# Kernel optimization log

Hardware: AMD Instinct MI355X
Metric: run time of the kernel (lower is better)

Reference implementation:

```python
import jax, jax.numpy as jnp
import numpy as np


def setup_inputs() -> dict:
    key = jax.random.key(0)
    kq, kk, kv = jax.random.split(key, 3)
    B, L, H, E = 2, 2048, 16, 64
    queries = jax.random.normal(kq, (B, L, H, E), dtype=jnp.float32)
    keys = jax.random.normal(kk, (B, L, H, E), dtype=jnp.float32)
    values = jax.random.normal(kv, (B, L, H, E), dtype=jnp.float32)
    return {"queries": queries, "keys": keys, "values": values}


def reference(queries, keys, values):
    # queries: [B, L, H, E], keys: [B, S, H, E], values: [B, S, H, D]
    B, L, H, E = queries.shape
    S = keys.shape[1]
    scale = 1.0 / jnp.sqrt(jnp.asarray(E, dtype=queries.dtype))
    # scores: [B, H, L, S]
    scores = jnp.einsum('blhe,bshe->bhls', queries, keys)
    # TriangularCausalMask: mask out strictly-upper-triangular (future) positions
    causal = jnp.triu(jnp.ones((L, S), dtype=bool), k=1)
    neg_inf = jnp.asarray(-jnp.inf, dtype=scores.dtype)
    scores = jnp.where(causal[None, None, :, :], neg_inf, scores)
    A = jax.nn.softmax(scale * scores, axis=-1)  # dropout p=0.0 (eval)
    # V: [B, L, H, D]
    V = jnp.einsum('bhls,bshd->blhd', A, values)
    return V
```

## Files before the change

kernel.cpp:

```cpp
#include <hip/hip_runtime.h>


constexpr int LL = 2048, HH = 16;
constexpr float SL2E = 0.125f * 1.44269504088896340736f;
constexpr float NEG = -1e30f;
constexpr size_t PLANE = 262144;

using bf16x8 = __attribute__((ext_vector_type(8))) short;
using f32x4  = __attribute__((ext_vector_type(4))) float;

__device__ inline float fast_exp2(float x) { return __builtin_amdgcn_exp2f(x); }

__device__ inline unsigned short f2bf(float f) {
    unsigned u = __builtin_bit_cast(unsigned, f);
    return (unsigned short)((u + 0x7fffu + ((u >> 16) & 1u)) >> 16);
}
__device__ inline unsigned pk2r(float lo, float hi) {
    unsigned al = __builtin_bit_cast(unsigned, lo) + 0x8000u;
    unsigned ah = __builtin_bit_cast(unsigned, hi) + 0x8000u;
    return __builtin_amdgcn_perm(ah, al, 0x07060302u);
}
__device__ inline void gload16(const void* g, void* l) {
    __builtin_amdgcn_global_load_lds(
        (const __attribute__((address_space(1))) unsigned int*)g,
        (__attribute__((address_space(3))) unsigned int*)l, 16, 0, 0);
}

__global__ __launch_bounds__(256) void prepack(
    const float* __restrict__ K, const float* __restrict__ V,
    char* __restrict__ wsK, char* __restrict__ wsV)
{
    const int bh = blockIdx.x >> 4;
    const int chunk = blockIdx.x & 15;
    const int b = bh >> 4, h = bh & 15;
    const int s0 = chunk * 128;
    const int tid = threadIdx.x;
    const int wv = tid >> 6, lane = tid & 63;
    const int g = lane >> 4, c16 = lane & 15;

    char* outK = wsK + (size_t)bh * PLANE;
    char* outV = wsV + (size_t)bh * PLANE;

    #pragma unroll
    for (int i = 0; i < 4; ++i) {
        const int idx = i * 256 + tid;
        const int sl = idx >> 3, o = idx & 7;
        const float* src = K + (((size_t)(b * 2048 + s0 + sl)) * 16 + h) * 64 + o * 8;
        float4 f0 = *(const float4*)src;
        float4 f1 = *(const float4*)(src + 4);
        short4 lo = make_short4((short)f2bf(f0.x), (short)f2bf(f0.y),
                                (short)f2bf(f0.z), (short)f2bf(f0.w));
        short4 hi = make_short4((short)f2bf(f1.x), (short)f2bf(f1.y),
                                (short)f2bf(f1.z), (short)f2bf(f1.w));
        char* dst = outK + (s0 + sl) * 128 + ((o << 4) ^ ((sl & 7) << 4));
        *(short4*)dst = lo;
        *(short4*)(dst + 8) = hi;
    }

    const int vrow0 = wv * 4 + g;
    const float* pV = V + (((size_t)(b * 2048 + s0 + vrow0)) * 16 + h) * 64 + c16 * 4;
    const int d = c16 * 4 + g;
    #pragma unroll
    for (int it = 0; it < 8; ++it) {
        float4 vf = *(const float4*)(pV + (size_t)it * 16 * 1024);
        unsigned short a0 = f2bf(vf.x), a1 = f2bf(vf.y),
                       a2 = f2bf(vf.z), a3 = f2bf(vf.w);
        unsigned s1 = (g & 1) ? ((unsigned)a0 | ((unsigned)a2 << 16))
                              : ((unsigned)a1 | ((unsigned)a3 << 16));
        unsigned r1 = __shfl_xor(s1, 16, 64);
        if (g & 1) { a0 = (unsigned short)r1; a2 = (unsigned short)(r1 >> 16); }
        else       { a1 = (unsigned short)r1; a3 = (unsigned short)(r1 >> 16); }
        unsigned s2 = (g & 2) ? ((unsigned)a0 | ((unsigned)a1 << 16))
                              : ((unsigned)a2 | ((unsigned)a3 << 16));
        unsigned r2 = __shfl_xor(s2, 32, 64);
        if (g & 2) { a0 = (unsigned short)r2; a1 = (unsigned short)(r2 >> 16); }
        else       { a2 = (unsigned short)r2; a3 = (unsigned short)(r2 >> 16); }
        const int p_g  = 4 * (it >> 1) + wv;
        const int half = it & 1;
        char* dst = outV + (size_t)d * 4096 + chunk * 256
                  + (((p_g ^ (d & 7)) << 4) + (half << 3));
        *(short4*)dst = make_short4((short)a0, (short)a1, (short)a2, (short)a3);
    }
}

__global__ __launch_bounds__(256, 2) void attn_main(
    const float* __restrict__ Q, const char* __restrict__ wsK,
    const char* __restrict__ wsV, float* __restrict__ Out)
{
    __shared__ __align__(16) short Kb[2][8192];
    __shared__ __align__(16) short Vt[2][8192];

    const int tid  = threadIdx.x;
    const int wv   = tid >> 6;
    const int lane = tid & 63;
    const int g    = lane >> 4;
    const int c16  = lane & 15;
    const int wq   = wv >> 1;
    const int wk   = wv & 1;

    const int i  = blockIdx.x;
    const int bh = ((i & 7) << 2) | ((i >> 3) & 3);
    const int qslot = i >> 5;
    const int qi = (qslot < 8) ? (15 - qslot) : (qslot - 8);
    const int b = bh >> 4, h = bh & 15;
    const int q0  = qi * 128;
    const int wqb = q0 + wq * 64;

    bf16x8 bQ[4][2];
    #pragma unroll
    for (int qg = 0; qg < 4; ++qg) {
        const int qrow = wqb + qg * 16 + c16;
        const float* qp = Q + ((size_t)(b * LL + qrow) * HH + h) * 64 + g * 8;
        #pragma unroll
        for (int es = 0; es < 2; ++es) {
            float4 f0 = *(const float4*)(qp + es * 32);
            float4 f1 = *(const float4*)(qp + es * 32 + 4);
            bf16x8 a;
            a[0] = f2bf(f0.x * SL2E); a[1] = f2bf(f0.y * SL2E);
            a[2] = f2bf(f0.z * SL2E); a[3] = f2bf(f0.w * SL2E);
            a[4] = f2bf(f1.x * SL2E); a[5] = f2bf(f1.y * SL2E);
            a[6] = f2bf(f1.z * SL2E); a[7] = f2bf(f1.w * SL2E);
            bQ[qg][es] = a;
        }
    }

    const short ONE = (short)0x3F80;
    const bf16x8 bOnes = {ONE, ONE, ONE, ONE, ONE, ONE, ONE, ONE};

    const char* planeK = wsK + (size_t)bh * PLANE;
    const char* planeV = wsV + (size_t)bh * PLANE;

    f32x4 Oacc[4][4];
    #pragma unroll
    for (int qg = 0; qg < 4; ++qg)
        #pragma unroll
        for (int dt = 0; dt < 4; ++dt) Oacc[qg][dt] = (f32x4){0.f, 0.f, 0.f, 0.f};
    f32x4 Lacc[4];
    #pragma unroll
    for (int qg = 0; qg < 4; ++qg) Lacc[qg] = (f32x4){0.f, 0.f, 0.f, 0.f};

    const int ntiles = qi + 1;

    auto stage = [&](int bi, int t) {
        const char* srcK = planeK + (size_t)t * 16384 + wv * 4096 + lane * 16;
        char* dstK = (char*)&Kb[bi][0] + wv * 4096;
        #pragma unroll
        for (int k = 0; k < 4; ++k)
            gload16(srcK + k * 1024, dstK + k * 1024);
        #pragma unroll
        for (int k = 0; k < 4; ++k) {
            const int ii = wv * 4 + k;
            const char* srcV = planeV + (size_t)(4 * ii + (lane >> 4)) * 4096
                             + (size_t)t * 256 + (lane & 15) * 16;
            gload16(srcV, (char*)&Vt[bi][0] + ii * 1024);
        }
    };

    int buf = 0;
    stage(0, 0);
    for (int t = 0; t < ntiles; ++t) {
        __syncthreads();
        if (t + 1 < ntiles) stage(buf ^ 1, t + 1);

        bf16x8 aK[4][2];
        #pragma unroll
        for (int kt2 = 0; kt2 < 4; ++kt2) {
            const int krow = (4 * wk + kt2) * 16 + c16;
            #pragma unroll
            for (int es = 0; es < 2; ++es) {
                const int off = krow * 128 + (((es * 64) + g * 16) ^ ((krow & 7) << 4));
                aK[kt2][es] = *(const bf16x8*)((char*)&Kb[buf][0] + off);
            }
        }
        bf16x8 bV[2][4];
        #pragma unroll
        for (int ksl = 0; ksl < 2; ++ksl) {
            const int ks = 2 * wk + ksl;
            #pragma unroll
            for (int dt = 0; dt < 4; ++dt) {
                const int d = dt * 16 + c16;
                const int voff = d * 256 + ((64 * ks + 16 * g) ^ ((d & 7) << 4));
                bV[ksl][dt] = *(const bf16x8*)((char*)&Vt[buf][0] + voff);
            }
        }

        const bool dia = (t == qi);
        #pragma unroll
        for (int qg = 0; qg < 4; ++qg) {
            f32x4 Sv[4];
            __builtin_amdgcn_s_setprio(1);
            #pragma unroll
            for (int kt2 = 0; kt2 < 4; ++kt2) {
                f32x4 acc = (f32x4){0.f, 0.f, 0.f, 0.f};
                acc = __builtin_amdgcn_mfma_f32_16x16x32_bf16(aK[kt2][0], bQ[qg][0], acc, 0, 0, 0);
                acc = __builtin_amdgcn_mfma_f32_16x16x32_bf16(aK[kt2][1], bQ[qg][1], acc, 0, 0, 0);
                Sv[kt2] = acc;
            }
            __builtin_amdgcn_s_setprio(0);

            const int thr = wq * 64 + qg * 16 + c16;
            unsigned pb[8];
            #pragma unroll
            for (int kt2 = 0; kt2 < 4; ++kt2) {
                float x0 = Sv[kt2][0], x1 = Sv[kt2][1];
                float x2 = Sv[kt2][2], x3 = Sv[kt2][3];
                if (dia) {
                    const int k0 = (4 * wk + kt2) * 16 + 4 * g;
                    x0 = (k0 + 0 <= thr) ? x0 : NEG;
                    x1 = (k0 + 1 <= thr) ? x1 : NEG;
                    x2 = (k0 + 2 <= thr) ? x2 : NEG;
                    x3 = (k0 + 3 <= thr) ? x3 : NEG;
                }
                const float p0 = fast_exp2(x0), p1 = fast_exp2(x1);
                const float p2 = fast_exp2(x2), p3 = fast_exp2(x3);
                pb[2 * kt2]     = pk2r(p0, p1);
                pb[2 * kt2 + 1] = pk2r(p2, p3);
            }

            __builtin_amdgcn_s_setprio(1);
            #pragma unroll
            for (int ksl = 0; ksl < 2; ++ksl) {
                uint4 u;
                u.x = pb[4 * ksl]; u.y = pb[4 * ksl + 1];
                u.z = pb[4 * ksl + 2]; u.w = pb[4 * ksl + 3];
                const bf16x8 pa = __builtin_bit_cast(bf16x8, u);
                Lacc[qg] = __builtin_amdgcn_mfma_f32_16x16x32_bf16(pa, bOnes, Lacc[qg], 0, 0, 0);
                #pragma unroll
                for (int dt = 0; dt < 4; ++dt)
                    Oacc[qg][dt] = __builtin_amdgcn_mfma_f32_16x16x32_bf16(pa, bV[ksl][dt], Oacc[qg][dt], 0, 0, 0);
            }
            __builtin_amdgcn_s_setprio(0);
        }
        buf ^= 1;
    }

    __syncthreads();
    float* Ko = (float*)&Kb[0][0];
    float* Lo = (float*)&Vt[0][0];
    if (wk) {
        #pragma unroll
        for (int qg = 0; qg < 4; ++qg) {
            #pragma unroll
            for (int dt = 0; dt < 4; ++dt) {
                const int idx = wq * 4096 + ((((qg * 4 + g) * 4 + dt) * 16 + c16) << 2);
                *(f32x4*)&Ko[idx] = Oacc[qg][dt];
            }
            if (c16 == 0)
                *(f32x4*)&Lo[wq * 64 + qg * 16 + g * 4] = Lacc[qg];
        }
    }
    __syncthreads();
    if (!wk) {
        #pragma unroll
        for (int qg = 0; qg < 4; ++qg) {
            const f32x4 lp = *(const f32x4*)&Lo[wq * 64 + qg * 16 + g * 4];
            Lacc[qg] += lp;
            #pragma unroll
            for (int dt = 0; dt < 4; ++dt) {
                const int idx = wq * 4096 + ((((qg * 4 + g) * 4 + dt) * 16 + c16) << 2);
                Oacc[qg][dt] += *(const f32x4*)&Ko[idx];
            }
            #pragma unroll
            for (int r = 0; r < 4; ++r) {
                const float inv = 1.0f / Lacc[qg][r];
                const int orow = q0 + wq * 64 + qg * 16 + g * 4 + r;
                float* op = Out + ((size_t)(b * LL + orow) * HH + h) * 64 + c16;
                #pragma unroll
                for (int dt = 0; dt < 4; ++dt)
                    op[dt * 16] = Oacc[qg][dt][r] * inv;
            }
        }
    }
}

extern "C" void kernel_launch(void* const* d_in, const int* in_sizes, int n_in,
                              void* d_out, int out_size, void* d_ws, size_t ws_size,
                              hipStream_t stream) {
    const float* Q = (const float*)d_in[0];
    const float* K = (const float*)d_in[1];
    const float* V = (const float*)d_in[2];
    float* out = (float*)d_out;
    (void)in_sizes; (void)n_in; (void)out_size; (void)ws_size;

    char* wsK = (char*)d_ws;
    char* wsV = (char*)d_ws + 32 * PLANE;
    prepack<<<512, 256, 0, stream>>>(K, V, wsK, wsV);
    attn_main<<<512, 256, 0, stream>>>(Q, wsK, wsV, out);
}
```

Measured before the change: 50.06 us.

## Pair causal q-tiles per block and split keys across four waves

Each block now handles two query tiles in sequence (a long one, 15-p, then a short one, p), so every block gets the same amount of causal work. The grid shrinks to 256 blocks of 512 threads. Keys are split over four waves instead of two, giving more waves per block and fewer registers per wave. The partial outputs and row sums are combined through shared memory in a staged tree reduction, which adds several barriers and more shared-memory traffic per tile.

```diff
diff --git a/kernel.cpp b/kernel.cpp
--- a/kernel.cpp
+++ b/kernel.cpp
@@ -83,191 +83,214 @@
     }
 }
 
-__global__ __launch_bounds__(256, 2) void attn_main(
+__global__ __launch_bounds__(512, 2) void attn_main(
     const float* __restrict__ Q, const char* __restrict__ wsK,
     const char* __restrict__ wsV, float* __restrict__ Out)
 {
-    __shared__ __align__(16) short Kb[2][8192];
-    __shared__ __align__(16) short Vt[2][8192];
+    __shared__ __align__(16) short Sh[32768];
+    char* ShB = (char*)&Sh[0];
 
     const int tid  = threadIdx.x;
     const int wv   = tid >> 6;
     const int lane = tid & 63;
     const int g    = lane >> 4;
     const int c16  = lane & 15;
-    const int wq   = wv >> 1;
-    const int wk   = wv & 1;
+    const int wq   = wv >> 2;
+    const int wk   = wv & 3;
 
     const int i  = blockIdx.x;
     const int bh = ((i & 7) << 2) | ((i >> 3) & 3);
-    const int qslot = i >> 5;
-    const int qi = (qslot < 8) ? (15 - qslot) : (qslot - 8);
+    const int p  = i >> 5;
     const int b = bh >> 4, h = bh & 15;
-    const int q0  = qi * 128;
-    const int wqb = q0 + wq * 64;
-
-    bf16x8 bQ[4][2];
-    #pragma unroll
-    for (int qg = 0; qg < 4; ++qg) {
-        const int qrow = wqb + qg * 16 + c16;
-        const float* qp = Q + ((size_t)(b * LL + qrow) * HH + h) * 64 + g * 8;
-        #pragma unroll
-        for (int es = 0; es < 2; ++es) {
-            float4 f0 = *(const float4*)(qp + es * 32);
-            float4 f1 = *(const float4*)(qp + es * 32 + 4);
-            bf16x8 a;
-            a[0] = f2bf(f0.x * SL2E); a[1] = f2bf(f0.y * SL2E);
-            a[2] = f2bf(f0.z * SL2E); a[3] = f2bf(f0.w * SL2E);
-            a[4] = f2bf(f1.x * SL2E); a[5] = f2bf(f1.y * SL2E);
-            a[6] = f2bf(f1.z * SL2E); a[7] = f2bf(f1.w * SL2E);
-            bQ[qg][es] = a;
-        }
-    }
+
+    const char* planeK = wsK + (size_t)bh * PLANE;
+    const char* planeV = wsV + (size_t)bh * PLANE;
 
     const short ONE = (short)0x3F80;
     const bf16x8 bOnes = {ONE, ONE, ONE, ONE, ONE, ONE, ONE, ONE};
 
-    const char* planeK = wsK + (size_t)bh * PLANE;
-    const char* planeV = wsV + (size_t)bh * PLANE;
-
-    f32x4 Oacc[4][4];
-    #pragma unroll
-    for (int qg = 0; qg < 4; ++qg)
-        #pragma unroll
-        for (int dt = 0; dt < 4; ++dt) Oacc[qg][dt] = (f32x4){0.f, 0.f, 0.f, 0.f};
-    f32x4 Lacc[4];
-    #pragma unroll
-    for (int qg = 0; qg < 4; ++qg) Lacc[qg] = (f32x4){0.f, 0.f, 0.f, 0.f};
-
-    const int ntiles = qi + 1;
-
     auto stage = [&](int bi, int t) {
-        const char* srcK = planeK + (size_t)t * 16384 + wv * 4096 + lane * 16;
-        char* dstK = (char*)&Kb[bi][0] + wv * 4096;
-        #pragma unroll
-        for (int k = 0; k < 4; ++k)
-            gload16(srcK + k * 1024, dstK + k * 1024);
-        #pragma unroll
-        for (int k = 0; k < 4; ++k) {
-            const int ii = wv * 4 + k;
-            const char* srcV = planeV + (size_t)(4 * ii + (lane >> 4)) * 4096
-                             + (size_t)t * 256 + (lane & 15) * 16;
-            gload16(srcV, (char*)&Vt[bi][0] + ii * 1024);
+        char* dK = ShB + bi * 16384;
+        char* dV = ShB + 32768 + bi * 16384;
+        #pragma unroll
+        for (int r = 0; r < 2; ++r) {
+            const int off = r * 8192 + wv * 1024;
+            gload16(planeK + (size_t)t * 16384 + off + lane * 16, dK + off);
+        }
+        #pragma unroll
+        for (int r = 0; r < 2; ++r) {
+            const int off = r * 8192 + wv * 1024;
+            const int d = r * 32 + wv * 4 + (lane >> 4);
+            gload16(planeV + (size_t)d * 4096 + (size_t)t * 256 + (lane & 15) * 16,
+                    dV + off);
         }
     };
 
-    int buf = 0;
-    stage(0, 0);
-    for (int t = 0; t < ntiles; ++t) {
-        __syncthreads();
-        if (t + 1 < ntiles) stage(buf ^ 1, t + 1);
-
-        bf16x8 aK[4][2];
-        #pragma unroll
-        for (int kt2 = 0; kt2 < 4; ++kt2) {
-            const int krow = (4 * wk + kt2) * 16 + c16;
+    #pragma unroll 1
+    for (int phase = 0; phase < 2; ++phase) {
+        const int qi = phase == 0 ? (15 - p) : p;
+        const int q0 = qi * 128;
+        const int ntiles = qi + 1;
+
+        bf16x8 bQ[4][2];
+        #pragma unroll
+        for (int qg = 0; qg < 4; ++qg) {
+            const int qrow = q0 + wq * 64 + qg * 16 + c16;
+            const float* qp = Q + ((size_t)(b * LL + qrow) * HH + h) * 64 + g * 8;
             #pragma unroll
             for (int es = 0; es < 2; ++es) {
-                const int off = krow * 128 + (((es * 64) + g * 16) ^ ((krow & 7) << 4));
-                aK[kt2][es] = *(const bf16x8*)((char*)&Kb[buf][0] + off);
-            }
-        }
-        bf16x8 bV[2][4];
-        #pragma unroll
-        for (int ksl = 0; ksl < 2; ++ksl) {
-            const int ks = 2 * wk + ksl;
+                float4 f0 = *(const float4*)(qp + es * 32);
+                float4 f1 = *(const float4*)(qp + es * 32 + 4);
+                bf16x8 a;
+                a[0] = f2bf(f0.x * SL2E); a[1] = f2bf(f0.y * SL2E);
+                a[2] = f2bf(f0.z * SL2E); a[3] = f2bf(f0.w * SL2E);
+                a[4] = f2bf(f1.x * SL2E); a[5] = f2bf(f1.y * SL2E);
+                a[6] = f2bf(f1.z * SL2E); a[7] = f2bf(f1.w * SL2E);
+                bQ[qg][es] = a;
+            }
+        }
+
+        f32x4 Oacc[4][4];
+        #pragma unroll
+        for (int qg = 0; qg < 4; ++qg)
+            #pragma unroll
+            for (int dt = 0; dt < 4; ++dt) Oacc[qg][dt] = (f32x4){0.f, 0.f, 0.f, 0.f};
+        f32x4 Lacc[4];
+        #pragma unroll
+        for (int qg = 0; qg < 4; ++qg) Lacc[qg] = (f32x4){0.f, 0.f, 0.f, 0.f};
+
+        if (phase) __syncthreads();
+        int buf = 0;
+        stage(0, 0);
+        for (int t = 0; t < ntiles; ++t) {
+            __syncthreads();
+            if (t + 1 < ntiles) stage(buf ^ 1, t + 1);
+
+            const char* Kbuf = ShB + buf * 16384;
+            const char* Vbuf = ShB + 32768 + buf * 16384;
+
+            bf16x8 aK[2][2];
+            #pragma unroll
+            for (int kt2 = 0; kt2 < 2; ++kt2) {
+                const int krow = (2 * wk + kt2) * 16 + c16;
+                #pragma unroll
+                for (int es = 0; es < 2; ++es) {
+                    const int off = krow * 128 + (((es * 64) + g * 16) ^ ((krow & 7) << 4));
+                    aK[kt2][es] = *(const bf16x8*)(Kbuf + off);
+                }
+            }
+            bf16x8 bV[4];
             #pragma unroll
             for (int dt = 0; dt < 4; ++dt) {
                 const int d = dt * 16 + c16;
-                const int voff = d * 256 + ((64 * ks + 16 * g) ^ ((d & 7) << 4));
-                bV[ksl][dt] = *(const bf16x8*)((char*)&Vt[buf][0] + voff);
-            }
-        }
-
-        const bool dia = (t == qi);
-        #pragma unroll
-        for (int qg = 0; qg < 4; ++qg) {
-            f32x4 Sv[4];
-            __builtin_amdgcn_s_setprio(1);
-            #pragma unroll
-            for (int kt2 = 0; kt2 < 4; ++kt2) {
-                f32x4 acc = (f32x4){0.f, 0.f, 0.f, 0.f};
-                acc = __builtin_amdgcn_mfma_f32_16x16x32_bf16(aK[kt2][0], bQ[qg][0], acc, 0, 0, 0);
-                acc = __builtin_amdgcn_mfma_f32_16x16x32_bf16(aK[kt2][1], bQ[qg][1], acc, 0, 0, 0);
-                Sv[kt2] = acc;
-            }
-            __builtin_amdgcn_s_setprio(0);
-
-            const int thr = wq * 64 + qg * 16 + c16;
-            unsigned pb[8];
-            #pragma unroll
-            for (int kt2 = 0; kt2 < 4; ++kt2) {
-                float x0 = Sv[kt2][0], x1 = Sv[kt2][1];
-                float x2 = Sv[kt2][2], x3 = Sv[kt2][3];
-                if (dia) {
-                    const int k0 = (4 * wk + kt2) * 16 + 4 * g;
-                    x0 = (k0 + 0 <= thr) ? x0 : NEG;
-                    x1 = (k0 + 1 <= thr) ? x1 : NEG;
-                    x2 = (k0 + 2 <= thr) ? x2 : NEG;
-                    x3 = (k0 + 3 <= thr) ? x3 : NEG;
+                const int voff = d * 256 + ((64 * wk + 16 * g) ^ ((d & 7) << 4));
+                bV[dt] = *(const bf16x8*)(Vbuf + voff);
+            }
+
+            const bool dia = (t == qi);
+            #pragma unroll
+            for (int qg = 0; qg < 4; ++qg) {
+                f32x4 Sv[2];
+                __builtin_amdgcn_s_setprio(1);
+                #pragma unroll
+                for (int kt2 = 0; kt2 < 2; ++kt2) {
+                    f32x4 acc = (f32x4){0.f, 0.f, 0.f, 0.f};
+                    acc = __builtin_amdgcn_mfma_f32_16x16x32_bf16(aK[kt2][0], bQ[qg][0], acc, 0, 0, 0);
+                    acc = __builtin_amdgcn_mfma_f32_16x16x32_bf16(aK[kt2][1], bQ[qg][1], acc, 0, 0, 0);
+                    Sv[kt2] = acc;
                 }
-                const float p0 = fast_exp2(x0), p1 = fast_exp2(x1);
-                const float p2 = fast_exp2(x2), p3 = fast_exp2(x3);
-                pb[2 * kt2]     = pk2r(p0, p1);
-                pb[2 * kt2 + 1] = pk2r(p2, p3);
-            }
-
-            __builtin_amdgcn_s_setprio(1);
-            #pragma unroll
-            for (int ksl = 0; ksl < 2; ++ksl) {
-                uint4 u;
-                u.x = pb[4 * ksl]; u.y = pb[4 * ksl + 1];
-                u.z = pb[4 * ksl + 2]; u.w = pb[4 * ksl + 3];
+                __builtin_amdgcn_s_setprio(0);
+
+                const int thr = wq * 64 + qg * 16 + c16;
+                unsigned pb[4];
+                #pragma unroll
+                for (int kt2 = 0; kt2 < 2; ++kt2) {
+                    float x0 = Sv[kt2][0], x1 = Sv[kt2][1];
+                    float x2 = Sv[kt2][2], x3 = Sv[kt2][3];
+                    if (dia) {
+                        const int k0 = (2 * wk + kt2) * 16 + 4 * g;
+                        x0 = (k0 + 0 <= thr) ? x0 : NEG;
+                        x1 = (k0 + 1 <= thr) ? x1 : NEG;
+                        x2 = (k0 + 2 <= thr) ? x2 : NEG;
+                        x3 = (k0 + 3 <= thr) ? x3 : NEG;
+                    }
+                    const float p0 = fast_exp2(x0), p1 = fast_exp2(x1);
+                    const float p2 = fast_exp2(x2), p3 = fast_exp2(x3);
+                    pb[2 * kt2]     = pk2r(p0, p1);
+                    pb[2 * kt2 + 1] = pk2r(p2, p3);
+                }
+
+                uint4 u; u.x = pb[0]; u.y = pb[1]; u.z = pb[2]; u.w = pb[3];
                 const bf16x8 pa = __builtin_bit_cast(bf16x8, u);
+                __builtin_amdgcn_s_setprio(1);
                 Lacc[qg] = __builtin_amdgcn_mfma_f32_16x16x32_bf16(pa, bOnes, Lacc[qg], 0, 0, 0);
                 #pragma unroll
                 for (int dt = 0; dt < 4; ++dt)
-                    Oacc[qg][dt] = __builtin_amdgcn_mfma_f32_16x16x32_bf16(pa, bV[ksl][dt], Oacc[qg][dt], 0, 0, 0);
-            }
-            __builtin_amdgcn_s_setprio(0);
-        }
-        buf ^= 1;
-    }
-
-    __syncthreads();
-    float* Ko = (float*)&Kb[0][0];
-    float* Lo = (float*)&Vt[0][0];
-    if (wk) {
-        #pragma unroll
-        for (int qg = 0; qg < 4; ++qg) {
-            #pragma unroll
-            for (int dt = 0; dt < 4; ++dt) {
-                const int idx = wq * 4096 + ((((qg * 4 + g) * 4 + dt) * 16 + c16) << 2);
-                *(f32x4*)&Ko[idx] = Oacc[qg][dt];
-            }
-            if (c16 == 0)
-                *(f32x4*)&Lo[wq * 64 + qg * 16 + g * 4] = Lacc[qg];
-        }
-    }
-    __syncthreads();
-    if (!wk) {
-        #pragma unroll
-        for (int qg = 0; qg < 4; ++qg) {
-            const f32x4 lp = *(const f32x4*)&Lo[wq * 64 + qg * 16 + g * 4];
-            Lacc[qg] += lp;
-            #pragma unroll
-            for (int dt = 0; dt < 4; ++dt) {
-                const int idx = wq * 4096 + ((((qg * 4 + g) * 4 + dt) * 16 + c16) << 2);
-                Oacc[qg][dt] += *(const f32x4*)&Ko[idx];
-            }
-            #pragma unroll
-            for (int r = 0; r < 4; ++r) {
-                const float inv = 1.0f / Lacc[qg][r];
-                const int orow = q0 + wq * 64 + qg * 16 + g * 4 + r;
-                float* op = Out + ((size_t)(b * LL + orow) * HH + h) * 64 + c16;
-                #pragma unroll
-                for (int dt = 0; dt < 4; ++dt)
-                    op[dt * 16] = Oacc[qg][dt][r] * inv;
+                    Oacc[qg][dt] = __builtin_amdgcn_mfma_f32_16x16x32_bf16(pa, bV[dt], Oacc[qg][dt], 0, 0, 0);
+                __builtin_amdgcn_s_setprio(0);
+            }
+            buf ^= 1;
+        }
+
+        __syncthreads();
+        float* Lr = (float*)ShB;
+        if (c16 == 0) {
+            #pragma unroll
+            for (int qg = 0; qg < 4; ++qg)
+                *(f32x4*)&Lr[wv * 64 + qg * 16 + g * 4] = Lacc[qg];
+        }
+        __syncthreads();
+        if (wk == 0) {
+            #pragma unroll
+            for (int qg = 0; qg < 4; ++qg)
+                #pragma unroll
+                for (int w2 = 1; w2 < 4; ++w2)
+                    Lacc[qg] += *(const f32x4*)&Lr[(wq * 4 + w2) * 64 + qg * 16 + g * 4];
+        }
+        __syncthreads();
+        if (wk >= 2) {
+            char* sp = ShB + (wq * 2 + (wk - 2)) * 16384;
+            #pragma unroll
+            for (int qg = 0; qg < 4; ++qg)
+                #pragma unroll
+                for (int dt = 0; dt < 4; ++dt)
+                    *(f32x4*)(sp + (((qg * 4 + g) * 4 + dt) * 16 + c16) * 16) = Oacc[qg][dt];
+        }
+        __syncthreads();
+        if (wk < 2) {
+            const char* sp = ShB + (wq * 2 + wk) * 16384;
+            #pragma unroll
+            for (int qg = 0; qg < 4; ++qg)
+                #pragma unroll
+                for (int dt = 0; dt < 4; ++dt)
+                    Oacc[qg][dt] += *(const f32x4*)(sp + (((qg * 4 + g) * 4 + dt) * 16 + c16) * 16);
+        }
+        __syncthreads();
+        if (wk == 1) {
+            char* sp = ShB + wq * 16384;
+            #pragma unroll
+            for (int qg = 0; qg < 4; ++qg)
+                #pragma unroll
+                for (int dt = 0; dt < 4; ++dt)
+                    *(f32x4*)(sp + (((qg * 4 + g) * 4 + dt) * 16 + c16) * 16) = Oacc[qg][dt];
+        }
+        __syncthreads();
+        if (wk == 0) {
+            const char* sp = ShB + wq * 16384;
+            #pragma unroll
+            for (int qg = 0; qg < 4; ++qg) {
+                #pragma unroll
+                for (int dt = 0; dt < 4; ++dt)
+                    Oacc[qg][dt] += *(const f32x4*)(sp + (((qg * 4 + g) * 4 + dt) * 16 + c16) * 16);
+                #pragma unroll
+                for (int r = 0; r < 4; ++r) {
+                    const float inv = 1.0f / Lacc[qg][r];
+                    const int orow = q0 + wq * 64 + qg * 16 + g * 4 + r;
+                    float* op = Out + ((size_t)(b * LL + orow) * HH + h) * 64 + c16;
+                    #pragma unroll
+                    for (int dt = 0; dt < 4; ++dt)
+                        op[dt * 16] = Oacc[qg][dt][r] * inv;
+                }
             }
         }
     }
@@ -285,5 +308,5 @@
     char* wsK = (char*)d_ws;
     char* wsV = (char*)d_ws + 32 * PLANE;
     prepack<<<512, 256, 0, stream>>>(K, V, wsK, wsV);
-    attn_main<<<512, 256, 0, stream>>>(Q, wsK, wsV, out);
-}
+    attn_main<<<256, 512, 0, stream>>>(Q, wsK, wsV, out);
+}
```

After: 49.91 us. Within noise of the previous version (-0.3%).
